# Optimization experiments

Hardware: AMD Instinct MI355X
Metric: run time of the kernel (lower is better)

## Reference

```python
import jax, jax.numpy as jnp
import numpy as np

NHID, NHEAD, HEAD_DIM, AL = 256, 10, 10, 2


def conv1x1(t, w, b):
    # t: [B, Cin, H, W], w: [Cout, Cin], b: [Cout]  (1x1 Conv2d)
    return jnp.einsum('bchw,oc->bohw', t, w) + b[None, :, None, None]


def setup_inputs() -> dict:
    key = jax.random.key(0)
    ks = jax.random.split(key, 12)
    B, L = 4, 2048
    d = NHEAD * HEAD_DIM  # 100
    sc_in = 1.0 / np.sqrt(NHID)
    sc_att = 1.0 / np.sqrt(3 * d)
    return {
        'x': jax.random.normal(ks[0], (B, NHID, L, 1), jnp.float32),
        'ax': jax.random.normal(ks[1], (B, NHID, AL, L), jnp.float32),
        'edge_matrix': jax.random.uniform(ks[2], (B, L, L), jnp.float32),
        'wq': jax.random.normal(ks[3], (d, NHID), jnp.float32) * sc_in,
        'bq': jnp.zeros((d,), jnp.float32),
        'wk': jax.random.normal(ks[4], (d, NHID), jnp.float32) * sc_in,
        'bk': jnp.zeros((d,), jnp.float32),
        'wv': jax.random.normal(ks[5], (d, NHID), jnp.float32) * sc_in,
        'bv': jnp.zeros((d,), jnp.float32),
        'wo': jax.random.normal(ks[6], (NHID, 3 * d), jnp.float32) * sc_att,
        'bo': jnp.zeros((NHID,), jnp.float32),
    }


def reference(x, ax, edge_matrix, wq, bq, wk, bk, wv, bv, wo, bo):
    B, _, L, _ = x.shape
    nh, hd = NHEAD, HEAD_DIM
    # NOTE: original torch code overwrites k and v with q (k=q.view, v=q.view),
    # so WK(x)/WV(x) are dead code; WK/WV are only applied to ax.
    q = conv1x1(x, wq, bq).reshape(B, nh, hd, 1, L)          # [B,nh,hd,1,L]
    ak = conv1x1(ax, wk, bk).reshape(B, nh, hd, AL, L)       # [B,nh,hd,aL,L]
    av = conv1x1(ax, wv, bv).reshape(B, nh, hd, AL, L)
    k = jnp.concatenate([q, ak], axis=3)                      # [B,nh,hd,1+aL,L]
    v = jnp.concatenate([q, av], axis=3)
    D = hd * (1 + AL)                                         # 30
    k = k.reshape(B, nh, D, L).transpose(0, 1, 3, 2)          # [B,nh,L,D]
    v = v.reshape(B, nh, D, L).transpose(0, 1, 3, 2)
    scores = jnp.einsum('bhld,bhmd->bhlm', k, v)              # [B,nh,L,L]
    alpha = jax.nn.softmax(scores * edge_matrix[:, None] / np.sqrt(hd), axis=-1)
    # dropout in eval mode (identity)
    att = jnp.einsum('bhlm,bhmd->bhld', alpha, v)             # [B,nh,L,D]
    # torch .view(B,-1,L,1) is a raw row-major reshape of the (B*nh,L,D) buffer
    att = att.reshape(B, nh * D, L, 1)
    return conv1x1(att, wo, bo)                               # [B,nhid,L,1]
```

## Files before the change

kernel.cpp:

```cpp
#include <hip/hip_runtime.h>
#include <hip/hip_bf16.h>
#include <math.h>

#define L 2048
#define NH 10
#define DP 32
#define D30 30

typedef __attribute__((ext_vector_type(8))) short bf16x8;
typedef __attribute__((ext_vector_type(4))) float f32x4;

__device__ inline short f2bf(float f) {
    union { float f; unsigned u; } v; v.f = f;
    unsigned r = (v.u + 0x7FFF + ((v.u >> 16) & 1)) >> 16;
    return (short)r;
}
__device__ inline unsigned pk2(float a, float b) {
    unsigned ua = __float_as_uint(a) + 0x8000u;
    unsigned ub = __float_as_uint(b) + 0x8000u;
    return (ua >> 16) | (ub & 0xFFFF0000u);
}
__device__ inline int permL(int l) {
    return (l & ~63) | ((l & 15) << 2) | ((l >> 4) & 3);
}

#define GLD16(g, l) __builtin_amdgcn_global_load_lds( \
    (__attribute__((address_space(1))) void*)(g),     \
    (__attribute__((address_space(3))) void*)(l), 16, 0, 0)

__global__ __launch_bounds__(256) void proj_kernel(
    const float* __restrict__ x, const float* __restrict__ ax,
    const float* __restrict__ wq, const float* __restrict__ bq,
    const float* __restrict__ wk, const float* __restrict__ bk,
    const float* __restrict__ wv, const float* __restrict__ bv,
    short* __restrict__ Kbuf, short* __restrict__ Vbuf, short* __restrict__ Vtbuf)
{
    __shared__ __align__(16) short Wl[112 * 72];
    __shared__ __align__(16) short XT[64 * 72];
    const int t  = threadIdx.x;
    const int l0 = blockIdx.x * 64;
    const int og = blockIdx.y;
    const int b  = blockIdx.z;

    const float* W; const float* bias;
    if (og == 0)      { W = wq; bias = bq; }
    else if (og <= 2) { W = wk; bias = bk; }
    else              { W = wv; bias = bv; }
    const int al = (og - 1) & 1;

    const int wid  = t >> 6;
    const int lane = t & 63;
    const int quad = lane >> 4;
    const int l15  = lane & 15;

    f32x4 acc[7];
    #pragma unroll
    for (int ot = 0; ot < 7; ot++) acc[ot] = (f32x4){0,0,0,0};

    const int cq = (t & 15) * 4;
    const int lq = (t >> 4) * 4;
    const size_t rs = (og == 0) ? (size_t)L : (size_t)(2 * L);

    for (int cc = 0; cc < 4; cc++) {
        const int c0 = cc * 64;
        __syncthreads();
        #pragma unroll
        for (int it = 0; it < 7; it++) {
            int kk = (t + it * 256) * 4;
            int o = kk >> 6, c = kk & 63;
            f32x4 v = {0, 0, 0, 0};
            if (o < 100) v = *(const f32x4*)(W + (size_t)o * 256 + c0 + c);
            uint2 u; u.x = pk2(v[0], v[1]); u.y = pk2(v[2], v[3]);
            *(uint2*)&Wl[o * 72 + c] = u;
        }
        {
            const float* src = (og == 0)
                ? x  + ((size_t)(b * 256 + c0 + cq)) * L + l0 + lq
                : ax + (((size_t)(b * 256 + c0 + cq)) * 2 + al) * L + l0 + lq;
            f32x4 r0 = *(const f32x4*)(src);
            f32x4 r1 = *(const f32x4*)(src + rs);
            f32x4 r2 = *(const f32x4*)(src + 2 * rs);
            f32x4 r3 = *(const f32x4*)(src + 3 * rs);
            #pragma unroll
            for (int i = 0; i < 4; i++) {
                uint2 u; u.x = pk2(r0[i], r1[i]); u.y = pk2(r2[i], r3[i]);
                *(uint2*)&XT[(lq + i) * 72 + cq] = u;
            }
        }
        __syncthreads();
        #pragma unroll
        for (int ks = 0; ks < 2; ks++) {
            bf16x8 bfrag = *(const bf16x8*)&XT[(wid * 16 + l15) * 72 + ks * 32 + quad * 8];
            #pragma unroll
            for (int ot = 0; ot < 7; ot++) {
                bf16x8 afrag = *(const bf16x8*)&Wl[(ot * 16 + l15) * 72 + ks * 32 + quad * 8];
                acc[ot] = __builtin_amdgcn_mfma_f32_16x16x32_bf16(afrag, bfrag, acc[ot], 0, 0, 0);
            }
        }
    }

    const int part = (og == 0) ? 0 : ((og == 1 || og == 3) ? 1 : 2);
    const float KS = 0.31622776601683794f * 1.4426950408889634f;
    const int l = l0 + wid * 16 + l15;
    #pragma unroll
    for (int ot = 0; ot < 7; ot++) {
        #pragma unroll
        for (int r = 0; r < 4; r++) {
            int o = ot * 16 + quad * 4 + r;
            if (o >= 100) continue;
            float val = acc[ot][r] + bias[o];
            int h = o / 10, dd = 3 * (o % 10) + part;
            size_t rowb = ((size_t)(b * NH + h)) * L;
            size_t tb   = ((size_t)(b * NH + h) * DP + dd) * L;
            if (og == 0) {
                Kbuf[(rowb + l) * DP + dd] = f2bf(val * KS);
                short s = f2bf(val);
                Vbuf[(rowb + l) * DP + dd] = s;
                Vtbuf[tb + permL(l)] = s;
            } else if (og <= 2) {
                Kbuf[(rowb + l) * DP + dd] = f2bf(val * KS);
            } else {
                short s = f2bf(val);
                Vbuf[(rowb + l) * DP + dd] = s;
                Vtbuf[tb + permL(l)] = s;
            }
        }
    }
}

__global__ __launch_bounds__(256, 4) void attn_kernel(
    const short* __restrict__ K, const short* __restrict__ V,
    const short* __restrict__ Vt, const float* __restrict__ edge,
    float* __restrict__ Opart, float* __restrict__ lsums, int npart)
{
    __shared__ __align__(16) short Vl[2][64 * 32];
    __shared__ __align__(16) short Vtl[2][32 * 64];
    __shared__ __align__(16) short Pm[4][2][16 * 72];
    const int t    = threadIdx.x;
    const int wid  = t >> 6;
    const int lane = t & 63;
    const int quad = lane >> 4;
    const int l15  = lane & 15;
    const int l0   = blockIdx.x * 64;
    const int h0   = blockIdx.y * 2;
    const int b    = blockIdx.z & 3;
    const int mz   = blockIdx.z >> 2;
    const size_t bh0 = (size_t)(b * NH + h0), bh1 = bh0 + 1;
    const int mbase = mz * (L / npart);
    const int nit   = (L / npart) / 64;

    const int lrow = l0 + wid * 16 + l15;
    bf16x8 kf0 = *(const bf16x8*)(K + (bh0 * L + lrow) * DP + quad * 8);
    bf16x8 kf1 = *(const bf16x8*)(K + (bh1 * L + lrow) * DP + quad * 8);

    const int myrow = l0 + wid * 16 + quad * 4;
    const float* e0 = edge + (size_t)b * L * L + (size_t)myrow * L + l15;

    float ls0[4] = {0, 0, 0, 0}, ls1[4] = {0, 0, 0, 0};
    f32x4 O00 = {0,0,0,0}, O01 = {0,0,0,0}, O10 = {0,0,0,0}, O11 = {0,0,0,0};
    const f32x4 z = {0,0,0,0};

    const int sh = wid & 1;
    const size_t sbh = bh0 + sh;

    for (int mt = 0; mt < nit; mt++) {
        const int m0 = mbase + mt * 64;
        __syncthreads();
        if (wid < 2) {
            const short* gb = V + (sbh * L + m0) * DP;
            #pragma unroll
            for (int k = 0; k < 4; k++) {
                int m = k * 16 + (lane >> 2);
                int g = (lane & 3) ^ ((lane >> 3) & 3);
                GLD16(gb + m * DP + g * 8, &Vl[sh][k * 16 * 32]);
            }
        } else {
            const short* gb = Vt + sbh * DP * L + m0;
            #pragma unroll
            for (int k = 0; k < 4; k++) {
                int d = k * 8 + (lane >> 3);
                int g = (lane & 7) ^ ((lane >> 3) & 7);
                GLD16(gb + (size_t)d * L + g * 8, &Vtl[sh][k * 8 * 64]);
            }
        }
        float e[4][4];
        #pragma unroll
        for (int r = 0; r < 4; r++)
            #pragma unroll
            for (int nb = 0; nb < 4; nb++)
                e[nb][r] = e0[(size_t)r * L + m0 + nb * 16];
        __syncthreads();

        f32x4 S0[4], S1[4];
        #pragma unroll
        for (int nb = 0; nb < 4; nb++) {
            int sw = (quad ^ ((l15 >> 1) & 3)) * 8;
            bf16x8 vf0 = *(const bf16x8*)&Vl[0][(nb * 16 + l15) * 32 + sw];
            bf16x8 vf1 = *(const bf16x8*)&Vl[1][(nb * 16 + l15) * 32 + sw];
            S0[nb] = __builtin_amdgcn_mfma_f32_16x16x32_bf16(kf0, vf0, z, 0, 0, 0);
            S1[nb] = __builtin_amdgcn_mfma_f32_16x16x32_bf16(kf1, vf1, z, 0, 0, 0);
        }

        short* P0 = &Pm[wid][0][0];
        short* P1 = &Pm[wid][1][0];
        #pragma unroll
        for (int r = 0; r < 4; r++) {
            float p0 = __builtin_amdgcn_exp2f(S0[0][r] * e[0][r]);
            float p1 = __builtin_amdgcn_exp2f(S0[1][r] * e[1][r]);
            float p2 = __builtin_amdgcn_exp2f(S0[2][r] * e[2][r]);
            float p3 = __builtin_amdgcn_exp2f(S0[3][r] * e[3][r]);
            ls0[r] += (p0 + p1) + (p2 + p3);
            uint2 u; u.x = pk2(p0, p1); u.y = pk2(p2, p3);
            *(uint2*)&P0[(quad * 4 + r) * 72 + l15 * 4] = u;
        }
        #pragma unroll
        for (int r = 0; r < 4; r++) {
            float p0 = __builtin_amdgcn_exp2f(S1[0][r] * e[0][r]);
            float p1 = __builtin_amdgcn_exp2f(S1[1][r] * e[1][r]);
            float p2 = __builtin_amdgcn_exp2f(S1[2][r] * e[2][r]);
            float p3 = __builtin_amdgcn_exp2f(S1[3][r] * e[3][r]);
            ls1[r] += (p0 + p1) + (p2 + p3);
            uint2 u; u.x = pk2(p0, p1); u.y = pk2(p2, p3);
            *(uint2*)&P1[(quad * 4 + r) * 72 + l15 * 4] = u;
        }

        #pragma unroll
        for (int ks = 0; ks < 2; ks++) {
            int G = ks * 4 + quad;
            int go = (G ^ (l15 & 7)) * 8;
            bf16x8 a0  = *(const bf16x8*)&P0[l15 * 72 + ks * 32 + quad * 8];
            bf16x8 b00 = *(const bf16x8*)&Vtl[0][l15 * 64 + go];
            bf16x8 b01 = *(const bf16x8*)&Vtl[0][(16 + l15) * 64 + go];
            O00 = __builtin_amdgcn_mfma_f32_16x16x32_bf16(a0, b00, O00, 0, 0, 0);
            O01 = __builtin_amdgcn_mfma_f32_16x16x32_bf16(a0, b01, O01, 0, 0, 0);
            bf16x8 a1  = *(const bf16x8*)&P1[l15 * 72 + ks * 32 + quad * 8];
            bf16x8 b10 = *(const bf16x8*)&Vtl[1][l15 * 64 + go];
            bf16x8 b11 = *(const bf16x8*)&Vtl[1][(16 + l15) * 64 + go];
            O10 = __builtin_amdgcn_mfma_f32_16x16x32_bf16(a1, b10, O10, 0, 0, 0);
            O11 = __builtin_amdgcn_mfma_f32_16x16x32_bf16(a1, b11, O11, 0, 0, 0);
        }
    }

    float* ab  = Opart + (size_t)mz * 2457600 + (size_t)b * 614400;
    float* lsp = lsums + (size_t)mz * 81920;
    #pragma unroll
    for (int r = 0; r < 4; r++) {
        float s0 = ls0[r];
        s0 += __shfl_xor(s0, 1); s0 += __shfl_xor(s0, 2);
        s0 += __shfl_xor(s0, 4); s0 += __shfl_xor(s0, 8);
        float s1 = ls1[r];
        s1 += __shfl_xor(s1, 1); s1 += __shfl_xor(s1, 2);
        s1 += __shfl_xor(s1, 4); s1 += __shfl_xor(s1, 8);
        int lr = myrow + r;
        if (l15 == 0) {
            lsp[bh0 * L + lr] = s0;
            lsp[bh1 * L + lr] = s1;
        }
        size_t base0 = (size_t)h0 * 61440 + (size_t)lr * D30;
        ab[base0 + l15] = O00[r];
        ab[base0 + 61440 + l15] = O10[r];
        if (l15 < 14) {
            ab[base0 + 16 + l15] = O01[r];
            ab[base0 + 61440 + 16 + l15] = O11[r];
        }
    }
}

__global__ __launch_bounds__(256) void combine_kernel(
    float* __restrict__ P0, const float* __restrict__ lsums, int npart)
{
    int i = blockIdx.x * 256 + threadIdx.x;
    float v = P0[i];
    int j = i / 30;
    float s = lsums[j];
    if (npart == 2) { v += P0[2457600 + i]; s += lsums[81920 + j]; }
    P0[i] = v / s;
}

__global__ __launch_bounds__(256) void wo16_kernel(
    const float* __restrict__ wo, short* __restrict__ wo16)
{
    int i4 = blockIdx.x * 256 + threadIdx.x;
    int idx = i4 * 4;
    int o = idx / 320, c = idx % 320;
    float v0 = (c + 0 < 300) ? wo[o * 300 + c + 0] : 0.f;
    float v1 = (c + 1 < 300) ? wo[o * 300 + c + 1] : 0.f;
    float v2 = (c + 2 < 300) ? wo[o * 300 + c + 2] : 0.f;
    float v3 = (c + 3 < 300) ? wo[o * 300 + c + 3] : 0.f;
    uint2 u; u.x = pk2(v0, v1); u.y = pk2(v2, v3);
    *(uint2*)&wo16[idx] = u;
}

__global__ __launch_bounds__(256, 4) void out_kernel(
    const float* __restrict__ ab4, const short* __restrict__ wo16,
    const float* __restrict__ bo, float* __restrict__ out)
{
    __shared__ __align__(16) short XT[32 * 72];
    const int t    = threadIdx.x;
    const int wid  = t >> 6;
    const int lane = t & 63;
    const int quad = lane >> 4;
    const int l15  = lane & 15;
    const int m0 = blockIdx.x * 32;
    const int o0 = blockIdx.y * 64;
    const int b  = blockIdx.z;
    const float* ab = ab4 + (size_t)b * 614400;

    f32x4 acc0 = {0,0,0,0}, acc1 = {0,0,0,0};
    const int cb = t >> 4;
    const int mb = t & 15;

    const short* wrow = wo16 + (size_t)(o0 + wid * 16 + l15) * 320;

    for (int cc = 0; cc < 5; cc++) {
        const int c0 = cc * 64;
        __syncthreads();
        {
            int cr0 = c0 + cb * 4;
            float2 r0, r1, r2, r3;
            int a0i = cr0 + 0; a0i = a0i < 300 ? a0i : 299;
            int a1i = cr0 + 1; a1i = a1i < 300 ? a1i : 299;
            int a2i = cr0 + 2; a2i = a2i < 300 ? a2i : 299;
            int a3i = cr0 + 3; a3i = a3i < 300 ? a3i : 299;
            r0 = *(const float2*)(ab + (size_t)a0i * L + m0 + mb * 2);
            r1 = *(const float2*)(ab + (size_t)a1i * L + m0 + mb * 2);
            r2 = *(const float2*)(ab + (size_t)a2i * L + m0 + mb * 2);
            r3 = *(const float2*)(ab + (size_t)a3i * L + m0 + mb * 2);
            uint2 u0; u0.x = pk2(r0.x, r1.x); u0.y = pk2(r2.x, r3.x);
            *(uint2*)&XT[(mb * 2 + 0) * 72 + cb * 4] = u0;
            uint2 u1; u1.x = pk2(r0.y, r1.y); u1.y = pk2(r2.y, r3.y);
            *(uint2*)&XT[(mb * 2 + 1) * 72 + cb * 4] = u1;
        }
        __syncthreads();
        #pragma unroll
        for (int ks = 0; ks < 2; ks++) {
            bf16x8 a  = *(const bf16x8*)(wrow + c0 + ks * 32 + quad * 8);
            bf16x8 b0 = *(const bf16x8*)&XT[l15 * 72 + ks * 32 + quad * 8];
            bf16x8 b1 = *(const bf16x8*)&XT[(16 + l15) * 72 + ks * 32 + quad * 8];
            acc0 = __builtin_amdgcn_mfma_f32_16x16x32_bf16(a, b0, acc0, 0, 0, 0);
            acc1 = __builtin_amdgcn_mfma_f32_16x16x32_bf16(a, b1, acc1, 0, 0, 0);
        }
    }
    #pragma unroll
    for (int r = 0; r < 4; r++) {
        int o = o0 + wid * 16 + quad * 4 + r;
        float bb = bo[o];
        float* orow = out + ((size_t)(b * 256 + o)) * L;
        orow[m0 + l15]      = acc0[r] + bb;
        orow[m0 + 16 + l15] = acc1[r] + bb;
    }
}

extern "C" void kernel_launch(void* const* d_in, const int* in_sizes, int n_in,
                              void* d_out, int out_size, void* d_ws, size_t ws_size,
                              hipStream_t stream) {
    const float* x    = (const float*)d_in[0];
    const float* ax   = (const float*)d_in[1];
    const float* edge = (const float*)d_in[2];
    const float* wq   = (const float*)d_in[3];
    const float* bq   = (const float*)d_in[4];
    const float* wk   = (const float*)d_in[5];
    const float* bk   = (const float*)d_in[6];
    const float* wv   = (const float*)d_in[7];
    const float* bv   = (const float*)d_in[8];
    const float* wo   = (const float*)d_in[9];
    const float* bo   = (const float*)d_in[10];
    float* out = (float*)d_out;

    const size_t KB  = (size_t)4 * NH * L * DP * 2;
    const size_t PSZ = (size_t)2457600 * 4;
    const size_t LSZ = (size_t)81920 * 4;
    const size_t WOS = (size_t)256 * 320 * 2;
    char* ws = (char*)d_ws;
    short* Kbuf  = (short*)ws;
    short* Vbuf  = (short*)(ws + KB);
    short* Vtbuf = (short*)(ws + 2 * KB);
    float* P0    = (float*)(ws + 3 * KB);
    int npart = (ws_size >= 3 * KB + 2 * PSZ + 2 * LSZ + WOS) ? 2 : 1;
    float* lsums = (float*)(ws + 3 * KB + (size_t)npart * PSZ);
    short* wo16  = (short*)(ws + 3 * KB + (size_t)npart * (PSZ + LSZ));
    if (ws_size < 3 * KB + PSZ + LSZ + WOS) return;

    hipMemsetAsync(ws, 0, 3 * KB, stream);

    wo16_kernel<<<dim3(80), 256, 0, stream>>>(wo, wo16);
    proj_kernel<<<dim3(32, 5, 4), 256, 0, stream>>>(x, ax, wq, bq, wk, bk, wv, bv,
                                                    Kbuf, Vbuf, Vtbuf);
    attn_kernel<<<dim3(32, 5, 4 * npart), 256, 0, stream>>>(Kbuf, Vbuf, Vtbuf, edge,
                                                            P0, lsums, npart);
    combine_kernel<<<dim3(9600), 256, 0, stream>>>(P0, lsums, npart);
    out_kernel<<<dim3(64, 4, 4), 256, 0, stream>>>(P0, wo16, bo, out);
}
```

Before: 229.2 us.

## Fuse combine into out_kernel, fold wo16 into proj, remap attention grid

```diff
diff --git a/kernel.cpp b/kernel.cpp
--- a/kernel.cpp
+++ b/kernel.cpp
@@ -33,14 +33,31 @@
     const float* __restrict__ wq, const float* __restrict__ bq,
     const float* __restrict__ wk, const float* __restrict__ bk,
     const float* __restrict__ wv, const float* __restrict__ bv,
+    const float* __restrict__ wo, short* __restrict__ wo16,
     short* __restrict__ Kbuf, short* __restrict__ Vbuf, short* __restrict__ Vtbuf)
 {
+    const int t  = threadIdx.x;
+    const int og = blockIdx.y;
+    const int b  = blockIdx.z;
+
+    if (og == 5) {
+        int id = (b * 32 + blockIdx.x) * 256 + t;
+        if (id < 20480) {
+            int idx = id * 4;
+            int o = idx / 320, c = idx % 320;
+            float v0 = (c + 0 < 300) ? wo[o * 300 + c + 0] : 0.f;
+            float v1 = (c + 1 < 300) ? wo[o * 300 + c + 1] : 0.f;
+            float v2 = (c + 2 < 300) ? wo[o * 300 + c + 2] : 0.f;
+            float v3 = (c + 3 < 300) ? wo[o * 300 + c + 3] : 0.f;
+            uint2 u; u.x = pk2(v0, v1); u.y = pk2(v2, v3);
+            *(uint2*)&wo16[idx] = u;
+        }
+        return;
+    }
+
     __shared__ __align__(16) short Wl[112 * 72];
     __shared__ __align__(16) short XT[64 * 72];
-    const int t  = threadIdx.x;
     const int l0 = blockIdx.x * 64;
-    const int og = blockIdx.y;
-    const int b  = blockIdx.z;
 
     const float* W; const float* bias;
     if (og == 0)      { W = wq; bias = bq; }
@@ -128,172 +145,141 @@
     }
 }
 
-__global__ __launch_bounds__(256, 4) void attn_kernel(
+__global__ __launch_bounds__(256, 5) void attn_kernel(
     const short* __restrict__ K, const short* __restrict__ V,
     const short* __restrict__ Vt, const float* __restrict__ edge,
     float* __restrict__ Opart, float* __restrict__ lsums, int npart)
 {
     __shared__ __align__(16) short Vl[2][64 * 32];
     __shared__ __align__(16) short Vtl[2][32 * 64];
-    __shared__ __align__(16) short Pm[4][2][16 * 72];
+    __shared__ __align__(16) short Pm[4][16 * 72];
     const int t    = threadIdx.x;
     const int wid  = t >> 6;
     const int lane = t & 63;
     const int quad = lane >> 4;
     const int l15  = lane & 15;
-    const int l0   = blockIdx.x * 64;
-    const int h0   = blockIdx.y * 2;
-    const int b    = blockIdx.z & 3;
-    const int mz   = blockIdx.z >> 2;
+
+    const int id  = blockIdx.x;
+    const int gg  = id / 40;
+    const int rem = id - gg * 40;
+    const int h2  = rem >> 3;
+    const int g   = gg * 8 + (rem & 7);
+    const int lb  = g & 31;
+    const int b   = (g >> 5) & 3;
+    const int mz  = g >> 7;
+
+    const int l0 = lb * 64;
+    const int h0 = h2 * 2;
     const size_t bh0 = (size_t)(b * NH + h0), bh1 = bh0 + 1;
     const int mbase = mz * (L / npart);
     const int nit   = (L / npart) / 64;
 
     const int lrow = l0 + wid * 16 + l15;
-    bf16x8 kf0 = *(const bf16x8*)(K + (bh0 * L + lrow) * DP + quad * 8);
-    bf16x8 kf1 = *(const bf16x8*)(K + (bh1 * L + lrow) * DP + quad * 8);
+    bf16x8 kf[2];
+    kf[0] = *(const bf16x8*)(K + (bh0 * L + lrow) * DP + quad * 8);
+    kf[1] = *(const bf16x8*)(K + (bh1 * L + lrow) * DP + quad * 8);
 
     const int myrow = l0 + wid * 16 + quad * 4;
-    const float* e0 = edge + (size_t)b * L * L + (size_t)myrow * L + l15;
-
-    float ls0[4] = {0, 0, 0, 0}, ls1[4] = {0, 0, 0, 0};
-    f32x4 O00 = {0,0,0,0}, O01 = {0,0,0,0}, O10 = {0,0,0,0}, O11 = {0,0,0,0};
-    const f32x4 z = {0,0,0,0};
+    const float* ep[4];
+    #pragma unroll
+    for (int r = 0; r < 4; r++)
+        ep[r] = edge + (size_t)b * L * L + (size_t)(myrow + r) * L + l15 + mbase;
 
     const int sh = wid & 1;
     const size_t sbh = bh0 + sh;
+    const short* sgp;
+    if (wid < 2)
+        sgp = V + (sbh * L + mbase + (lane >> 2)) * DP + (((lane & 3) ^ ((lane >> 3) & 3)) * 8);
+    else
+        sgp = Vt + (sbh * DP + (lane >> 3)) * L + mbase + (((lane & 7) ^ ((lane >> 3) & 7)) * 8);
+
+    float ls[2][4] = {{0,0,0,0},{0,0,0,0}};
+    f32x4 O[2][2] = {{{0,0,0,0},{0,0,0,0}},{{0,0,0,0},{0,0,0,0}}};
+    const f32x4 z = {0,0,0,0};
 
     for (int mt = 0; mt < nit; mt++) {
-        const int m0 = mbase + mt * 64;
         __syncthreads();
         if (wid < 2) {
-            const short* gb = V + (sbh * L + m0) * DP;
-            #pragma unroll
-            for (int k = 0; k < 4; k++) {
-                int m = k * 16 + (lane >> 2);
-                int g = (lane & 3) ^ ((lane >> 3) & 3);
-                GLD16(gb + m * DP + g * 8, &Vl[sh][k * 16 * 32]);
-            }
+            #pragma unroll
+            for (int k = 0; k < 4; k++)
+                GLD16(sgp + k * (16 * DP), &Vl[sh][k * 512]);
         } else {
-            const short* gb = Vt + sbh * DP * L + m0;
-            #pragma unroll
-            for (int k = 0; k < 4; k++) {
-                int d = k * 8 + (lane >> 3);
-                int g = (lane & 7) ^ ((lane >> 3) & 7);
-                GLD16(gb + (size_t)d * L + g * 8, &Vtl[sh][k * 8 * 64]);
-            }
+            #pragma unroll
+            for (int k = 0; k < 4; k++)
+                GLD16(sgp + (size_t)k * (8 * L), &Vtl[sh][k * 512]);
         }
         float e[4][4];
         #pragma unroll
         for (int r = 0; r < 4; r++)
             #pragma unroll
             for (int nb = 0; nb < 4; nb++)
-                e[nb][r] = e0[(size_t)r * L + m0 + nb * 16];
-        __syncthreads();
-
-        f32x4 S0[4], S1[4];
-        #pragma unroll
-        for (int nb = 0; nb < 4; nb++) {
-            int sw = (quad ^ ((l15 >> 1) & 3)) * 8;
-            bf16x8 vf0 = *(const bf16x8*)&Vl[0][(nb * 16 + l15) * 32 + sw];
-            bf16x8 vf1 = *(const bf16x8*)&Vl[1][(nb * 16 + l15) * 32 + sw];
-            S0[nb] = __builtin_amdgcn_mfma_f32_16x16x32_bf16(kf0, vf0, z, 0, 0, 0);
-            S1[nb] = __builtin_amdgcn_mfma_f32_16x16x32_bf16(kf1, vf1, z, 0, 0, 0);
-        }
-
-        short* P0 = &Pm[wid][0][0];
-        short* P1 = &Pm[wid][1][0];
-        #pragma unroll
-        for (int r = 0; r < 4; r++) {
-            float p0 = __builtin_amdgcn_exp2f(S0[0][r] * e[0][r]);
-            float p1 = __builtin_amdgcn_exp2f(S0[1][r] * e[1][r]);
-            float p2 = __builtin_amdgcn_exp2f(S0[2][r] * e[2][r]);
-            float p3 = __builtin_amdgcn_exp2f(S0[3][r] * e[3][r]);
-            ls0[r] += (p0 + p1) + (p2 + p3);
-            uint2 u; u.x = pk2(p0, p1); u.y = pk2(p2, p3);
-            *(uint2*)&P0[(quad * 4 + r) * 72 + l15 * 4] = u;
-        }
-        #pragma unroll
-        for (int r = 0; r < 4; r++) {
-            float p0 = __builtin_amdgcn_exp2f(S1[0][r] * e[0][r]);
-            float p1 = __builtin_amdgcn_exp2f(S1[1][r] * e[1][r]);
-            float p2 = __builtin_amdgcn_exp2f(S1[2][r] * e[2][r]);
-            float p3 = __builtin_amdgcn_exp2f(S1[3][r] * e[3][r]);
-            ls1[r] += (p0 + p1) + (p2 + p3);
-            uint2 u; u.x = pk2(p0, p1); u.y = pk2(p2, p3);
-            *(uint2*)&P1[(quad * 4 + r) * 72 + l15 * 4] = u;
-        }
-
-        #pragma unroll
-        for (int ks = 0; ks < 2; ks++) {
-            int G = ks * 4 + quad;
-            int go = (G ^ (l15 & 7)) * 8;
-            bf16x8 a0  = *(const bf16x8*)&P0[l15 * 72 + ks * 32 + quad * 8];
-            bf16x8 b00 = *(const bf16x8*)&Vtl[0][l15 * 64 + go];
-            bf16x8 b01 = *(const bf16x8*)&Vtl[0][(16 + l15) * 64 + go];
-            O00 = __builtin_amdgcn_mfma_f32_16x16x32_bf16(a0, b00, O00, 0, 0, 0);
-            O01 = __builtin_amdgcn_mfma_f32_16x16x32_bf16(a0, b01, O01, 0, 0, 0);
-            bf16x8 a1  = *(const bf16x8*)&P1[l15 * 72 + ks * 32 + quad * 8];
-            bf16x8 b10 = *(const bf16x8*)&Vtl[1][l15 * 64 + go];
-            bf16x8 b11 = *(const bf16x8*)&Vtl[1][(16 + l15) * 64 + go];
-            O10 = __builtin_amdgcn_mfma_f32_16x16x32_bf16(a1, b10, O10, 0, 0, 0);
-            O11 = __builtin_amdgcn_mfma_f32_16x16x32_bf16(a1, b11, O11, 0, 0, 0);
-        }
+                e[nb][r] = ep[r][nb * 16];
+        __syncthreads();
+
+        short* P = &Pm[wid][0];
+        #pragma unroll
+        for (int hh = 0; hh < 2; hh++) {
+            f32x4 S[4];
+            #pragma unroll
+            for (int nb = 0; nb < 4; nb++) {
+                int sw = (quad ^ ((l15 >> 1) & 3)) * 8;
+                bf16x8 vf = *(const bf16x8*)&Vl[hh][(nb * 16 + l15) * 32 + sw];
+                S[nb] = __builtin_amdgcn_mfma_f32_16x16x32_bf16(kf[hh], vf, z, 0, 0, 0);
+            }
+            #pragma unroll
+            for (int r = 0; r < 4; r++) {
+                float p0 = __builtin_amdgcn_exp2f(S[0][r] * e[0][r]);
+                float p1 = __builtin_amdgcn_exp2f(S[1][r] * e[1][r]);
+                float p2 = __builtin_amdgcn_exp2f(S[2][r] * e[2][r]);
+                float p3 = __builtin_amdgcn_exp2f(S[3][r] * e[3][r]);
+                ls[hh][r] += (p0 + p1) + (p2 + p3);
+                uint2 u; u.x = pk2(p0, p1); u.y = pk2(p2, p3);
+                *(uint2*)&P[(quad * 4 + r) * 72 + l15 * 4] = u;
+            }
+            #pragma unroll
+            for (int ks = 0; ks < 2; ks++) {
+                int go = ((ks * 4 + quad) ^ (l15 & 7)) * 8;
+                bf16x8 a  = *(const bf16x8*)&P[l15 * 72 + ks * 32 + quad * 8];
+                bf16x8 b0 = *(const bf16x8*)&Vtl[hh][l15 * 64 + go];
+                bf16x8 b1 = *(const bf16x8*)&Vtl[hh][(16 + l15) * 64 + go];
+                O[hh][0] = __builtin_amdgcn_mfma_f32_16x16x32_bf16(a, b0, O[hh][0], 0, 0, 0);
+                O[hh][1] = __builtin_amdgcn_mfma_f32_16x16x32_bf16(a, b1, O[hh][1], 0, 0, 0);
+            }
+        }
+        #pragma unroll
+        for (int r = 0; r < 4; r++) ep[r] += 64;
+        sgp += (wid < 2) ? 64 * DP : 64;
     }
 
     float* ab  = Opart + (size_t)mz * 2457600 + (size_t)b * 614400;
-    float* lsp = lsums + (size_t)mz * 81920;
+    float* lsp = lsums + (size_t)mz * 81920 + (size_t)b * 20480;
     #pragma unroll
     for (int r = 0; r < 4; r++) {
-        float s0 = ls0[r];
+        float s0 = ls[0][r];
         s0 += __shfl_xor(s0, 1); s0 += __shfl_xor(s0, 2);
         s0 += __shfl_xor(s0, 4); s0 += __shfl_xor(s0, 8);
-        float s1 = ls1[r];
+        float s1 = ls[1][r];
         s1 += __shfl_xor(s1, 1); s1 += __shfl_xor(s1, 2);
         s1 += __shfl_xor(s1, 4); s1 += __shfl_xor(s1, 8);
         int lr = myrow + r;
         if (l15 == 0) {
-            lsp[bh0 * L + lr] = s0;
-            lsp[bh1 * L + lr] = s1;
+            lsp[h0 * L + lr]       = s0;
+            lsp[(h0 + 1) * L + lr] = s1;
         }
         size_t base0 = (size_t)h0 * 61440 + (size_t)lr * D30;
-        ab[base0 + l15] = O00[r];
-        ab[base0 + 61440 + l15] = O10[r];
+        ab[base0 + l15]         = O[0][0][r];
+        ab[base0 + 61440 + l15] = O[1][0][r];
         if (l15 < 14) {
-            ab[base0 + 16 + l15] = O01[r];
-            ab[base0 + 61440 + 16 + l15] = O11[r];
-        }
-    }
-}
-
-__global__ __launch_bounds__(256) void combine_kernel(
-    float* __restrict__ P0, const float* __restrict__ lsums, int npart)
-{
-    int i = blockIdx.x * 256 + threadIdx.x;
-    float v = P0[i];
-    int j = i / 30;
-    float s = lsums[j];
-    if (npart == 2) { v += P0[2457600 + i]; s += lsums[81920 + j]; }
-    P0[i] = v / s;
-}
-
-__global__ __launch_bounds__(256) void wo16_kernel(
-    const float* __restrict__ wo, short* __restrict__ wo16)
-{
-    int i4 = blockIdx.x * 256 + threadIdx.x;
-    int idx = i4 * 4;
-    int o = idx / 320, c = idx % 320;
-    float v0 = (c + 0 < 300) ? wo[o * 300 + c + 0] : 0.f;
-    float v1 = (c + 1 < 300) ? wo[o * 300 + c + 1] : 0.f;
-    float v2 = (c + 2 < 300) ? wo[o * 300 + c + 2] : 0.f;
-    float v3 = (c + 3 < 300) ? wo[o * 300 + c + 3] : 0.f;
-    uint2 u; u.x = pk2(v0, v1); u.y = pk2(v2, v3);
-    *(uint2*)&wo16[idx] = u;
+            ab[base0 + 16 + l15]         = O[0][1][r];
+            ab[base0 + 61440 + 16 + l15] = O[1][1][r];
+        }
+    }
 }
 
 __global__ __launch_bounds__(256, 4) void out_kernel(
-    const float* __restrict__ ab4, const short* __restrict__ wo16,
-    const float* __restrict__ bo, float* __restrict__ out)
+    const float* __restrict__ Opart, const float* __restrict__ lsums,
+    const short* __restrict__ wo16, const float* __restrict__ bo,
+    float* __restrict__ out, int npart)
 {
     __shared__ __align__(16) short XT[32 * 72];
     const int t    = threadIdx.x;
@@ -304,31 +290,40 @@
     const int m0 = blockIdx.x * 32;
     const int o0 = blockIdx.y * 64;
     const int b  = blockIdx.z;
-    const float* ab = ab4 + (size_t)b * 614400;
+    const float* P0b = Opart + (size_t)b * 614400;
+    const float* P1b = Opart + 2457600 + (size_t)b * 614400;
+    const float* ls0 = lsums + (size_t)b * 20480;
+    const float* ls1 = lsums + 81920 + (size_t)b * 20480;
 
     f32x4 acc0 = {0,0,0,0}, acc1 = {0,0,0,0};
     const int cb = t >> 4;
     const int mb = t & 15;
-
     const short* wrow = wo16 + (size_t)(o0 + wid * 16 + l15) * 320;
 
     for (int cc = 0; cc < 5; cc++) {
         const int c0 = cc * 64;
         __syncthreads();
         {
-            int cr0 = c0 + cb * 4;
-            float2 r0, r1, r2, r3;
-            int a0i = cr0 + 0; a0i = a0i < 300 ? a0i : 299;
-            int a1i = cr0 + 1; a1i = a1i < 300 ? a1i : 299;
-            int a2i = cr0 + 2; a2i = a2i < 300 ? a2i : 299;
-            int a3i = cr0 + 3; a3i = a3i < 300 ? a3i : 299;
-            r0 = *(const float2*)(ab + (size_t)a0i * L + m0 + mb * 2);
-            r1 = *(const float2*)(ab + (size_t)a1i * L + m0 + mb * 2);
-            r2 = *(const float2*)(ab + (size_t)a2i * L + m0 + mb * 2);
-            r3 = *(const float2*)(ab + (size_t)a3i * L + m0 + mb * 2);
-            uint2 u0; u0.x = pk2(r0.x, r1.x); u0.y = pk2(r2.x, r3.x);
+            int crb = c0 + cb * 4;
+            float vx[4], vy[4];
+            #pragma unroll
+            for (int i = 0; i < 4; i++) {
+                int cr = crb + i; if (cr > 299) cr = 299;
+                int f = cr * 2048 + m0 + mb * 2;
+                float2 p = *(const float2*)(P0b + f);
+                int j0 = f / 30, j1 = (f + 1) / 30;
+                float s0 = ls0[j0], s1 = ls0[j1];
+                if (npart == 2) {
+                    float2 q = *(const float2*)(P1b + f);
+                    p.x += q.x; p.y += q.y;
+                    s0 += ls1[j0]; s1 += ls1[j1];
+                }
+                vx[i] = p.x * __builtin_amdgcn_rcpf(s0);
+                vy[i] = p.y * __builtin_amdgcn_rcpf(s1);
+            }
+            uint2 u0; u0.x = pk2(vx[0], vx[1]); u0.y = pk2(vx[2], vx[3]);
             *(uint2*)&XT[(mb * 2 + 0) * 72 + cb * 4] = u0;
-            uint2 u1; u1.x = pk2(r0.y, r1.y); u1.y = pk2(r2.y, r3.y);
+            uint2 u1; u1.x = pk2(vy[0], vy[1]); u1.y = pk2(vy[2], vy[3]);
             *(uint2*)&XT[(mb * 2 + 1) * 72 + cb * 4] = u1;
         }
         __syncthreads();
@@ -383,11 +378,9 @@
 
     hipMemsetAsync(ws, 0, 3 * KB, stream);
 
-    wo16_kernel<<<dim3(80), 256, 0, stream>>>(wo, wo16);
-    proj_kernel<<<dim3(32, 5, 4), 256, 0, stream>>>(x, ax, wq, bq, wk, bk, wv, bv,
-                                                    Kbuf, Vbuf, Vtbuf);
-    attn_kernel<<<dim3(32, 5, 4 * npart), 256, 0, stream>>>(Kbuf, Vbuf, Vtbuf, edge,
-                                                            P0, lsums, npart);
-    combine_kernel<<<dim3(9600), 256, 0, stream>>>(P0, lsums, npart);
-    out_kernel<<<dim3(64, 4, 4), 256, 0, stream>>>(P0, wo16, bo, out);
-}
+    proj_kernel<<<dim3(32, 6, 4), 256, 0, stream>>>(x, ax, wq, bq, wk, bk, wv, bv,
+                                                    wo, wo16, Kbuf, Vbuf, Vtbuf);
+    attn_kernel<<<dim3(640 * npart), 256, 0, stream>>>(Kbuf, Vbuf, Vtbuf, edge,
+                                                       P0, lsums, npart);
+    out_kernel<<<dim3(64, 4, 4), 256, 0, stream>>>(P0, lsums, wo16, bo, out, npart);
+}
```

After: 221.1 us. 1.04x faster.
